# Kernel optimization log

Measured on AMD Instinct MI355X. Metric: run time of the kernel, lower is better.

Reference implementation:

```python
import jax, jax.numpy as jnp
import numpy as np

B, R, L_, K_, U_, E = 16, 32, 64, 16, 4, 64  # batch, realizations, APs, users, antennas, embed dim
C2 = 2 * U_                                   # input_dim_2 == output_dim == 2U
EPS = 1e-5


def _uniform(key, shape, fan_out, fan_in):
    # matches torch init: U(-ini, ini) with ini = sqrt(3/(out*in))
    ini = float(np.sqrt(3.0 / (fan_out * fan_in)))
    return jax.random.uniform(key, shape, jnp.float32, -ini, ini)


def setup_inputs() -> dict:
    key = jax.random.key(0)
    ks = jax.random.split(key, 12)
    return {
        "Hhat_real": jax.random.normal(ks[0], (B, R, L_, K_, U_), jnp.float32),
        "Hhat_imag": jax.random.normal(ks[1], (B, R, L_, K_, U_), jnp.float32),
        # layer 0 (hidden, out=E) -- note P3/P5 exist in torch but are unused in forward
        "P1_0": _uniform(ks[2], (E, E), E, E),
        "P2_0": _uniform(ks[3], (E, E), E, E),
        "P4_0": _uniform(ks[4], (E, C2), E, C2),
        "g0": jnp.ones((E,), jnp.float32),
        "b0": jnp.zeros((E,), jnp.float32),
        # layer 1 (hidden, out=E)
        "P1_1": _uniform(ks[5], (E, E), E, E),
        "P2_1": _uniform(ks[6], (E, E), E, E),
        "P4_1": _uniform(ks[7], (E, C2), E, C2),
        "g1": jnp.ones((E,), jnp.float32),
        "b1": jnp.zeros((E,), jnp.float32),
        # layer 2 (output, out=2U, no BN / no ReLU)
        "P1_2": _uniform(ks[8], (C2, E), C2, E),
        "P2_2": _uniform(ks[9], (C2, E), C2, E),
        "P4_2": _uniform(ks[10], (C2, C2), C2, C2),
        "nbrOfRealizations": R,
        "L": L_,
        "K": K_,
        "U": U_,
    }


def _layer(A, H, P1, P2, P4, gamma, beta, is_last):
    # A: [BR, C1, L, K], H: [BR, C2, L, K]
    A1 = jnp.einsum('oc,bclk->bolk', P1, A)
    A2 = jnp.einsum('oc,bcl->bol', P2, A.mean(-1))[:, :, :, None]   # mean over K
    A3 = jnp.einsum('oc,bck->bok', P2, A.mean(-2))[:, :, None, :]   # mean over L
    A4 = jnp.einsum('oc,bcl->bol', P4, H.mean(-1))[:, :, :, None]
    A5 = jnp.einsum('oc,bck->bok', P4, H.mean(-2))[:, :, None, :]
    out = 2 * A1 + 2 * A2 + 2 * A3 + 0.1 * A4 + 0.1 * A5
    if is_last:
        return out
    out = jax.nn.relu(out)
    # BatchNorm2d, training mode: biased variance over (batch, L, K)
    mu = out.mean((0, 2, 3), keepdims=True)
    var = ((out - mu) ** 2).mean((0, 2, 3), keepdims=True)
    return (out - mu) / jnp.sqrt(var + EPS) * gamma[None, :, None, None] + beta[None, :, None, None]


def reference(Hhat_real, Hhat_imag, P1_0, P2_0, P4_0, g0, b0,
              P1_1, P2_1, P4_1, g1, b1, P1_2, P2_2, P4_2,
              nbrOfRealizations, L, K, U):
    batch = Hhat_real.shape[0]
    BR = batch * nbrOfRealizations
    # [B,R,L,K,U] -> [BR,U,L,K] (real / imag channels), concat -> [BR, 2U, L, K]
    Hr = Hhat_real.reshape(BR, L, K, U).transpose(0, 3, 1, 2)
    Hi = Hhat_imag.reshape(BR, L, K, U).transpose(0, 3, 1, 2)
    Hup = jnp.concatenate([Hr, Hi], axis=1)
    A = jnp.zeros((BR, E, L, K), jnp.float32)  # V_AP_updated init
    A = _layer(A, Hup, P1_0, P2_0, P4_0, g0, b0, False)
    A = _layer(A, Hup, P1_1, P2_1, P4_1, g1, b1, False)
    V = _layer(A, Hup, P1_2, P2_2, P4_2, None, None, True)  # [BR, 2U, L, K]
    V = V.reshape(BR, 2, U, L, K)
    F1 = jnp.transpose(V[:, 0], (0, 2, 3, 1))  # [BR, L, K, U]
    F2 = jnp.transpose(V[:, 1], (0, 2, 3, 1))
    norm = jnp.sqrt((F1 ** 2).sum(-1) + (F2 ** 2).sum(-1))[..., None]
    Fhat = (F1 + 1j * F2) / norm
    return Fhat.reshape(batch, nbrOfRealizations, L, K, U)
```

## Files before the change

kernel.cpp:

```cpp
#include <hip/hip_runtime.h>
#include <math.h>

#define BRR 512
#define LLL 64
#define KKK 16
#define EEE 64
#define CC2 8
#define PPP 1024
#define BN_EPS 1e-5f
#define NSTRIPE 16

__device__ __forceinline__ float relu_f(float v){ return v>0.f?v:0.f; }
__device__ __forceinline__ int lds_row(int r){ return r*68 + (((r>>3)&7)<<2); }

#define OFF_HBL  0u
#define OFF_HBK  262144u
#define OFF_Y0   327680u
#define OFF_X1   851968u
#define OFF_Y1   2949120u
#define OFF_X2   3473408u
#define OFF_Y2   3735552u
#define OFF_M1L  3801088u
#define OFF_M1K  5898240u
#define OFF_SUM0 6422528u
#define OFF_SSQ0 6423552u
#define OFF_SUM1 6424576u
#define OFF_SSQ1 6425600u
#define OFF_S0   6426624u
#define OFF_T0   6426688u
#define OFF_S1   6426752u
#define OFF_T1   6426816u
#define WS_FLOATS 6426880u
#define OFF_M1KB 6426880u
#define OFF_T1S  6951168u
#define WS_BIG   40505600u

__global__ void k_zero(float4* __restrict__ p, int n4){
  int t = blockIdx.x*256 + threadIdx.x;
  if (t < n4) p[t] = make_float4(0.f,0.f,0.f,0.f);
}

__global__ __launch_bounds__(256) void k_prep(const float* __restrict__ Hr,
                                              const float* __restrict__ Hi,
                                              const float* __restrict__ P40,
                                              float* __restrict__ ws){
  __shared__ float sm[9344];
  int b = blockIdx.x, tid = threadIdx.x;
  const float* hrg = Hr + (size_t)b*4096;
  const float* hig = Hi + (size_t)b*4096;
  for (int t=tid;t<4096;t+=256){ sm[t]=hrg[t]; sm[4096+t]=hig[t]; }
  for (int t=tid;t<512;t+=256){ int c=t&63,j=t>>6; sm[8192+j*64+c]=P40[c*8+j]; }
  __syncthreads();
  for (int t=tid;t<512;t+=256){ int l=t>>3,c2=t&7;
    const float* src=sm+((c2<4)?0:4096); int u=c2&3;
    float s=0.f;
    #pragma unroll
    for(int k=0;k<16;++k) s+=src[(l*16+k)*4+u];
    sm[8704+t]=s*(1.f/16.f); }
  for (int t=tid;t<128;t+=256){ int k=t>>3,c2=t&7;
    const float* src=sm+((c2<4)?0:4096); int u=c2&3;
    float s=0.f;
    for(int l=0;l<64;++l) s+=src[(l*16+k)*4+u];
    sm[9216+t]=s*(1.f/64.f); }
  __syncthreads();
  for (int t=tid;t<1024;t+=256){ int k=t>>6,c=t&63; float s=0.f;
    #pragma unroll
    for(int j=0;j<8;++j) s+=sm[8192+j*64+c]*sm[9216+k*8+j];
    sm[4096+t]=0.1f*s; }
  for (int t=tid;t<4096;t+=256){ int l=t>>6,c=t&63; float s=0.f;
    #pragma unroll
    for(int j=0;j<8;++j) s+=sm[8192+j*64+c]*sm[8704+l*8+j];
    sm[t]=0.1f*s; }
  __syncthreads();
  for (int t=tid;t<1024;t+=256){ int c=t&63; float yv=sm[4096+t]; float s=0.f;
    for(int l=0;l<64;++l) s+=relu_f(sm[l*64+c]+yv);
    sm[5120+t]=s*(1.f/64.f); }
  float ssum=0.f, ssq=0.f;
  for (int t=tid;t<4096;t+=256){ int c=t&63; float xv=sm[t]; float s=0.f;
    #pragma unroll
    for(int k=0;k<16;++k){ float v=relu_f(xv+sm[4096+k*64+c]); s+=v; ssq+=v*v; }
    ssum+=s;
    ws[OFF_X1+(size_t)b*4096+t]=s*(1.f/16.f); }
  __syncthreads();
  sm[6144+tid]=ssum; sm[6400+tid]=ssq;
  __syncthreads();
  if (tid<64){
    float ts =sm[6144+tid]+sm[6208+tid]+sm[6272+tid]+sm[6336+tid];
    float tss=sm[6400+tid]+sm[6464+tid]+sm[6528+tid]+sm[6592+tid];
    int stripe = b & (NSTRIPE-1);
    atomicAdd(&ws[OFF_SUM0+stripe*64+tid], ts);
    atomicAdd(&ws[OFF_SSQ0+stripe*64+tid], tss);
  }
  for (int t=tid;t<512;t+=256)  ws[OFF_HBL+(size_t)b*512+t]=sm[8704+t];
  for (int t=tid;t<128;t+=256)  ws[OFF_HBK+(size_t)b*128+t]=sm[9216+t];
  for (int t=tid;t<1024;t+=256) ws[OFF_Y0+(size_t)b*1024+t]=sm[4096+t];
  for (int t=tid;t<1024;t+=256) ws[OFF_Y1+(size_t)b*1024+t]=sm[5120+t];
  for (int t=tid;t<4096;t+=256) ws[OFF_M1L+(size_t)b*4096+t]=sm[t];
}

__global__ void k_bn(float* __restrict__ ws, const float* __restrict__ g_,
                     const float* __restrict__ b_, unsigned sumOff, unsigned outOff){
  int tid = threadIdx.x;
  if (tid < 64){
    float s=0.f, ss=0.f;
    for (int i=0;i<NSTRIPE;++i){ s+=ws[sumOff+i*64+tid]; ss+=ws[sumOff+1024+i*64+tid]; }
    const float invN = 1.0f/((float)BRR*LLL*KKK);
    float mu=s*invN, var=ss*invN-mu*mu;
    float sc = g_[tid]/sqrtf(var+BN_EPS);
    ws[outOff+tid]=sc;
    ws[outOff+64+tid]=b_[tid]-mu*sc;
  }
}

__global__ __launch_bounds__(256) void k_xy1(float* __restrict__ ws,
                                             const float* __restrict__ P21,
                                             const float* __restrict__ P41){
  __shared__ float wt[4096], p41[512], mrow[1024], hbs[128], s0l[64], t0l[64];
  int bx = blockIdx.x, tid = threadIdx.x;
  for (int t=tid;t<4096;t+=256) wt[t] = 2.0f*P21[(t&63)*64 + (t>>6)];
  for (int t=tid;t<512;t+=256)  p41[t] = P41[t];
  if (tid<64){ s0l[tid]=ws[OFF_S0+tid]; t0l[tid]=ws[OFF_T0+tid]; }
  bool isX = bx < 2048;
  int row0 = isX ? bx*16 : (bx-2048)*16;
  if (isX){
    for (int t=tid;t<1024;t+=256) mrow[t] = ws[OFF_X1+(size_t)row0*64+t];
    if (tid<128) hbs[tid] = ws[OFF_HBL+(size_t)row0*8+tid];
  } else {
    for (int t=tid;t<1024;t+=256) mrow[t] = ws[OFF_Y1+(size_t)row0*64+t];
    if (tid<128) hbs[tid] = ws[OFF_HBK+(size_t)row0*8+tid];
  }
  __syncthreads();
  for (int t=tid;t<1024;t+=256){ int c=t&63; mrow[t]=s0l[c]*mrow[t]+t0l[c]; }
  __syncthreads();
  int r4 = tid>>6, o = tid&63;
  #pragma unroll
  for (int rr=0;rr<4;++rr){
    int rl = rr*4 + r4;
    float s=0.f;
    for (int c=0;c<64;++c) s += wt[c*64+o]*mrow[rl*64+c];
    float s2=0.f;
    #pragma unroll
    for (int j=0;j<8;++j) s2 += p41[o*8+j]*hbs[rl*8+j];
    float res = s + 0.1f*s2;
    if (isX) ws[OFF_X1+(size_t)(row0+rl)*64+o] = res;
    else     ws[OFF_Y1+(size_t)(row0+rl)*64+o] = res;
  }
}

#define T_W1   0
#define T_X08  4384
#define T_Y0   4896
#define T_X1   5984
#define T_Y1   6496
#define T_S0   7520
#define T_T0   7584
#define T_P4T0 7648
#define T_HB8  8160
#define T_END  8224

__device__ void t1_tile(float* sm, const float* __restrict__ ws,
                        const float* __restrict__ P11, const float* __restrict__ P40,
                        int b, int pblk, int tid,
                        float acc[8][4], int og, int pg, int lloc, int c0){
  for (int t=tid;t<4096;t+=256){ int o=t>>6,c=t&63; sm[T_W1+lds_row(o)+c]=2.0f*P11[t]; }
  for (int t=tid;t<1024;t+=256){ int k=t>>6,c=t&63; sm[T_Y0+k*68+c]=ws[OFF_Y0+(size_t)b*1024+t]; }
  for (int t=tid;t<512;t+=256)  sm[T_X1+t]=ws[OFF_X1+((size_t)b*64+pblk*8)*64+t];
  for (int t=tid;t<1024;t+=256) sm[T_Y1+t]=ws[OFF_Y1+(size_t)b*1024+t];
  for (int t=tid;t<512;t+=256){ int c=t&63,j=t>>6; sm[T_P4T0+j*64+c]=P40[c*8+j]; }
  if (tid<64){ sm[T_S0+tid]=ws[OFF_S0+tid]; sm[T_T0+tid]=ws[OFF_T0+tid]; }
  else if (tid<128){ int t2=tid-64; sm[T_HB8+t2]=ws[OFF_HBL+((size_t)b*64+pblk*8)*8+t2]; }
  __syncthreads();
  for (int e=tid;e<512;e+=256){ int l=e>>6,c=e&63; float s=0.f;
    #pragma unroll
    for(int j=0;j<8;++j) s += sm[T_P4T0+j*64+c]*sm[T_HB8+l*8+j];
    sm[T_X08+e]=0.1f*s; }
  __syncthreads();
  {
    float xb[8];
    *(float4*)&xb[0] = *(const float4*)&sm[T_X1 + lloc*64 + c0];
    *(float4*)&xb[4] = *(const float4*)&sm[T_X1 + lloc*64 + c0 + 4];
    #pragma unroll
    for (int i=0;i<4;++i){
      int k=(pg&3)*4+i;
      float yb[8];
      *(float4*)&yb[0] = *(const float4*)&sm[T_Y1 + k*64 + c0];
      *(float4*)&yb[4] = *(const float4*)&sm[T_Y1 + k*64 + c0 + 4];
      #pragma unroll
      for (int j=0;j<8;++j) acc[j][i]=xb[j]+yb[j];
    }
  }
  #pragma unroll 4
  for (int c4=0;c4<16;++c4){
    float4 xr  = *(const float4*)&sm[T_X08 + lloc*64 + c4*4];
    float4 s0v = *(const float4*)&sm[T_S0 + c4*4];
    float4 t0v = *(const float4*)&sm[T_T0 + c4*4];
    float4 aa[4];
    #pragma unroll
    for (int i=0;i<4;++i){
      int k=(pg&3)*4+i;
      float4 yr = *(const float4*)&sm[T_Y0 + k*68 + c4*4];
      aa[i].x = s0v.x*relu_f(xr.x+yr.x)+t0v.x;
      aa[i].y = s0v.y*relu_f(xr.y+yr.y)+t0v.y;
      aa[i].z = s0v.z*relu_f(xr.z+yr.z)+t0v.z;
      aa[i].w = s0v.w*relu_f(xr.w+yr.w)+t0v.w;
    }
    #pragma unroll
    for (int j=0;j<8;++j){
      float4 w = *(const float4*)&sm[T_W1 + lds_row(c0+j) + c4*4];
      #pragma unroll
      for (int i=0;i<4;++i)
        acc[j][i] += w.x*aa[i].x + w.y*aa[i].y + w.z*aa[i].z + w.w*aa[i].w;
    }
  }
  #pragma unroll
  for (int j=0;j<8;++j)
    #pragma unroll
    for (int i=0;i<4;++i) acc[j][i] = relu_f(acc[j][i]);
}

#define PD_W1   0
#define PD_Y0   4384
#define PD_Y1   5472
#define PD_X1D  6496
#define PD_X08D 7520
#define PD_CT   8544
#define PD_S0   8608
#define PD_T0   8672
#define PD_TOT  8736

__global__ __launch_bounds__(256) void k_pass1e(float* __restrict__ ws,
                                                const float* __restrict__ P11){
  __shared__ float sm[PD_TOT];
  int b = blockIdx.x >> 1, h = blockIdx.x & 1;
  int pb0 = h*4;
  int tid=threadIdx.x;
  int og=tid&7, pg=tid>>3, lloc=pg>>2, kg=pg&3, c0=og*8, wv=tid>>6;
  for (int t4=tid;t4<1024;t4+=256){ int o=t4>>4,c=(t4&15)*4;
    float4 v = *(const float4*)&P11[o*64+c];
    v.x*=2.f; v.y*=2.f; v.z*=2.f; v.w*=2.f;
    *(float4*)&sm[PD_W1+lds_row(o)+c]=v; }
  for (int t4=tid;t4<256;t4+=256){ int k=t4>>4,c=(t4&15)*4;
    float4 v = *(const float4*)&ws[OFF_Y0+(size_t)b*1024+t4*4];
    (void)k;
    *(float4*)&sm[PD_Y0+(t4>>4)*68+((t4&15)*4)]=v; }
  for (int t4=tid;t4<256;t4+=256)
    *(float4*)&sm[PD_Y1+t4*4] = *(const float4*)&ws[OFF_Y1+(size_t)b*1024+t4*4];
  if (tid<64){ sm[PD_S0+tid]=ws[OFF_S0+tid]; sm[PD_T0+tid]=ws[OFF_T0+tid]; }
  __syncthreads();
  if (tid<64){
    float ct=0.f;
    for (int c=0;c<64;++c) ct += sm[PD_W1+lds_row(tid)+c]*sm[PD_T0+c];
    sm[PD_CT+tid]=ct;
  }
  __syncthreads();
  for (int t4=tid;t4<1024;t4+=256){ int o=t4>>4,c=(t4&15)*4;
    float4 w = *(float4*)&sm[PD_W1+lds_row(o)+c];
    float4 s = *(const float4*)&sm[PD_S0+c];
    w.x*=s.x; w.y*=s.y; w.z*=s.z; w.w*=s.w;
    *(float4*)&sm[PD_W1+lds_row(o)+c]=w; }
  if (tid<128){
    float4 v1 = *(const float4*)&ws[OFF_X1 +((size_t)b*64+pb0*8)*64 + (size_t)tid*4];
    float4 v8 = *(const float4*)&ws[OFF_M1L+((size_t)b*64+pb0*8)*64 + (size_t)tid*4];
    *(float4*)&sm[PD_X1D  + tid*4] = v1;
    *(float4*)&sm[PD_X08D + tid*4] = v8;
  }
  float qsum[8], mk[8][4];
  #pragma unroll
  for (int j=0;j<8;++j){ qsum[j]=0.f;
    #pragma unroll
    for (int i=0;i<4;++i) mk[j][i]=0.f; }
  #pragma unroll 1
  for (int pp=0;pp<4;++pp){
    int pblk = pb0+pp;
    __syncthreads();
    if (pp<3 && tid<128){
      int pn = pblk+1;
      float4 v1 = *(const float4*)&ws[OFF_X1 +((size_t)b*64+pn*8)*64 + (size_t)tid*4];
      float4 v8 = *(const float4*)&ws[OFF_M1L+((size_t)b*64+pn*8)*64 + (size_t)tid*4];
      int bo = ((pp+1)&1)*512;
      *(float4*)&sm[PD_X1D  + bo + tid*4] = v1;
      *(float4*)&sm[PD_X08D + bo + tid*4] = v8;
    }
    int cb = (pp&1)*512;
    float acc[8][4];
    {
      float xb[8], ctv[8];
      *(float4*)&xb[0]  = *(const float4*)&sm[PD_X1D + cb + lloc*64 + c0];
      *(float4*)&xb[4]  = *(const float4*)&sm[PD_X1D + cb + lloc*64 + c0 + 4];
      *(float4*)&ctv[0] = *(const float4*)&sm[PD_CT + c0];
      *(float4*)&ctv[4] = *(const float4*)&sm[PD_CT + c0 + 4];
      #pragma unroll
      for (int i=0;i<4;++i){
        int k=kg*4+i;
        float yb[8];
        *(float4*)&yb[0] = *(const float4*)&sm[PD_Y1 + k*64 + c0];
        *(float4*)&yb[4] = *(const float4*)&sm[PD_Y1 + k*64 + c0 + 4];
        #pragma unroll
        for (int j=0;j<8;++j) acc[j][i]=xb[j]+yb[j]+ctv[j];
      }
    }
    #pragma unroll 4
    for (int c4=0;c4<16;++c4){
      float4 xr = *(const float4*)&sm[PD_X08D + cb + lloc*64 + c4*4];
      float4 aa[4];
      #pragma unroll
      for (int i=0;i<4;++i){
        int k=kg*4+i;
        float4 yr = *(const float4*)&sm[PD_Y0 + k*68 + c4*4];
        aa[i].x = relu_f(xr.x+yr.x);
        aa[i].y = relu_f(xr.y+yr.y);
        aa[i].z = relu_f(xr.z+yr.z);
        aa[i].w = relu_f(xr.w+yr.w);
      }
      #pragma unroll
      for (int j=0;j<8;++j){
        float4 w = *(const float4*)&sm[PD_W1 + lds_row(c0+j) + c4*4];
        #pragma unroll
        for (int i=0;i<4;++i)
          acc[j][i] += w.x*aa[i].x + w.y*aa[i].y + w.z*aa[i].z + w.w*aa[i].w;
      }
    }
    #pragma unroll
    for (int j=0;j<8;++j)
      #pragma unroll
      for (int i=0;i<4;++i) acc[j][i] = relu_f(acc[j][i]);
    {
      size_t tbase = OFF_T1S + ((size_t)b*8 + pblk)*8192 + (size_t)tid*4;
      #pragma unroll
      for (int j=0;j<8;++j)
        *(float4*)&ws[tbase + j*1024] =
          make_float4(acc[j][0],acc[j][1],acc[j][2],acc[j][3]);
    }
    float sj[8];
    #pragma unroll
    for (int j=0;j<8;++j){
      sj[j]=acc[j][0]+acc[j][1]+acc[j][2]+acc[j][3];
      qsum[j]+=acc[j][0]*acc[j][0]+acc[j][1]*acc[j][1]+acc[j][2]*acc[j][2]+acc[j][3]*acc[j][3];
      #pragma unroll
      for (int i=0;i<4;++i) mk[j][i]+=acc[j][i];
    }
    #pragma unroll
    for (int j=0;j<8;++j){
      float r=sj[j];
      r += __shfl_xor(r, 8, 64);
      r += __shfl_xor(r, 16, 64);
      sj[j]=r;
    }
    if (kg==0){
      const float inv16 = 1.f/16.f;
      float4 v0 = make_float4(sj[0]*inv16, sj[1]*inv16, sj[2]*inv16, sj[3]*inv16);
      float4 v1 = make_float4(sj[4]*inv16, sj[5]*inv16, sj[6]*inv16, sj[7]*inv16);
      size_t base = OFF_M1L + ((size_t)b*64 + pblk*8 + lloc)*64 + c0;
      *(float4*)&ws[base]   = v0;
      *(float4*)&ws[base+4] = v1;
    }
  }
  __syncthreads();
  #pragma unroll
  for (int j=0;j<8;++j){
    #pragma unroll
    for (int i=0;i<4;++i){
      float v = mk[j][i] + __shfl_xor(mk[j][i], 32, 64);
      if ((tid & 32)==0)
        sm[wv*1088 + (og*4+kg)*33 + i*8 + j] = v;
    }
  }
  #pragma unroll
  for (int j=0;j<8;++j) sm[4384+(c0+j)*33+pg] = qsum[j];
  __syncthreads();
  unsigned mko = h ? OFF_M1KB : OFF_M1K;
  float tsacc=0.f;
  #pragma unroll
  for (int r=0;r<4;++r){
    int e = tid + r*256;
    int k=e>>6, c=e&63;
    int a = ((c>>3)*4+(k>>2))*33 + (k&3)*8 + (c&7);
    float v = sm[a]+sm[1088+a]+sm[2176+a]+sm[3264+a];
    tsacc += v;
    ws[mko+(size_t)b*1024+e] = v*(1.f/64.f);
  }
  sm[6496 + (tid&63)*5 + wv] = tsacc;
  __syncthreads();
  if (tid<64){
    float ts  = sm[6496+tid*5+0]+sm[6496+tid*5+1]+sm[6496+tid*5+2]+sm[6496+tid*5+3];
    float tss = 0.f;
    for (int g=0; g<32; ++g) tss += sm[4384+tid*33+g];
    int stripe = b & (NSTRIPE-1);
    atomicAdd(&ws[OFF_SUM1+stripe*64+tid], ts);
    atomicAdd(&ws[OFF_SSQ1+stripe*64+tid], tss);
  }
}

#define MK_OFF 8224
__global__ __launch_bounds__(256) void k_pass1(float* __restrict__ ws,
                                               const float* __restrict__ P11,
                                               const float* __restrict__ P40){
  __shared__ float sm[12576];
  int b=blockIdx.x, tid=threadIdx.x;
  int og=tid&7, pg=tid>>3, lloc=pg>>2, kg=pg&3, c0=og*8, wv=tid>>6;
  for (int t=tid;t<4096;t+=256){ int o=t>>6,c=t&63; sm[T_W1+lds_row(o)+c]=2.0f*P11[t]; }
  for (int t=tid;t<1024;t+=256){ int k=t>>6,c=t&63; sm[T_Y0+k*68+c]=ws[OFF_Y0+(size_t)b*1024+t]; }
  for (int t=tid;t<1024;t+=256) sm[T_Y1+t]=ws[OFF_Y1+(size_t)b*1024+t];
  for (int t=tid;t<512;t+=256){ int c=t&63,j=t>>6; sm[T_P4T0+j*64+c]=P40[c*8+j]; }
  if (tid<64){ sm[T_S0+tid]=ws[OFF_S0+tid]; sm[T_T0+tid]=ws[OFF_T0+tid]; }
  for (int t=tid;t<4352;t+=256) sm[MK_OFF+t]=0.f;
  float qsum[8];
  #pragma unroll
  for (int j=0;j<8;++j) qsum[j]=0.f;
  #pragma unroll 1
  for (int pblk=0;pblk<8;++pblk){
    __syncthreads();
    for (int t=tid;t<512;t+=256) sm[T_X1+t]=ws[OFF_X1+((size_t)b*64+pblk*8)*64+t];
    if (tid<64) sm[T_HB8+tid]=ws[OFF_HBL+((size_t)b*64+pblk*8)*8+tid];
    __syncthreads();
    for (int e=tid;e<512;e+=256){ int l=e>>6,c=e&63; float s=0.f;
      #pragma unroll
      for(int j=0;j<8;++j) s += sm[T_P4T0+j*64+c]*sm[T_HB8+l*8+j];
      sm[T_X08+e]=0.1f*s; }
    __syncthreads();
    float acc[8][4];
    {
      float xb[8];
      *(float4*)&xb[0] = *(const float4*)&sm[T_X1 + lloc*64 + c0];
      *(float4*)&xb[4] = *(const float4*)&sm[T_X1 + lloc*64 + c0 + 4];
      #pragma unroll
      for (int i=0;i<4;++i){
        int k=kg*4+i;
        float yb[8];
        *(float4*)&yb[0] = *(const float4*)&sm[T_Y1 + k*64 + c0];
        *(float4*)&yb[4] = *(const float4*)&sm[T_Y1 + k*64 + c0 + 4];
        #pragma unroll
        for (int j=0;j<8;++j) acc[j][i]=xb[j]+yb[j];
      }
    }
    #pragma unroll 4
    for (int c4=0;c4<16;++c4){
      float4 xr  = *(const float4*)&sm[T_X08 + lloc*64 + c4*4];
      float4 s0v = *(const float4*)&sm[T_S0 + c4*4];
      float4 t0v = *(const float4*)&sm[T_T0 + c4*4];
      float4 aa[4];
      #pragma unroll
      for (int i=0;i<4;++i){
        int k=kg*4+i;
        float4 yr = *(const float4*)&sm[T_Y0 + k*68 + c4*4];
        aa[i].x = s0v.x*relu_f(xr.x+yr.x)+t0v.x;
        aa[i].y = s0v.y*relu_f(xr.y+yr.y)+t0v.y;
        aa[i].z = s0v.z*relu_f(xr.z+yr.z)+t0v.z;
        aa[i].w = s0v.w*relu_f(xr.w+yr.w)+t0v.w;
      }
      #pragma unroll
      for (int j=0;j<8;++j){
        float4 w = *(const float4*)&sm[T_W1 + lds_row(c0+j) + c4*4];
        #pragma unroll
        for (int i=0;i<4;++i)
          acc[j][i] += w.x*aa[i].x + w.y*aa[i].y + w.z*aa[i].z + w.w*aa[i].w;
      }
    }
    #pragma unroll
    for (int j=0;j<8;++j)
      #pragma unroll
      for (int i=0;i<4;++i) acc[j][i] = relu_f(acc[j][i]);
    float sj[8];
    #pragma unroll
    for (int j=0;j<8;++j){
      sj[j]=acc[j][0]+acc[j][1]+acc[j][2]+acc[j][3];
      qsum[j]+=acc[j][0]*acc[j][0]+acc[j][1]*acc[j][1]+acc[j][2]*acc[j][2]+acc[j][3]*acc[j][3];
    }
    #pragma unroll
    for (int j=0;j<8;++j){
      float r=sj[j];
      r += __shfl_xor(r, 8, 64);
      r += __shfl_xor(r, 16, 64);
      sj[j]=r;
    }
    if (kg==0){
      const float inv16 = 1.f/16.f;
      float4 v0 = make_float4(sj[0]*inv16, sj[1]*inv16, sj[2]*inv16, sj[3]*inv16);
      float4 v1 = make_float4(sj[4]*inv16, sj[5]*inv16, sj[6]*inv16, sj[7]*inv16);
      size_t base = OFF_M1L + ((size_t)b*64 + pblk*8 + lloc)*64 + c0;
      *(float4*)&ws[base]   = v0;
      *(float4*)&ws[base+4] = v1;
    }
    #pragma unroll
    for (int j=0;j<8;++j){
      #pragma unroll
      for (int i=0;i<4;++i){
        float v = acc[j][i] + __shfl_xor(acc[j][i], 32, 64);
        if ((tid & 32)==0)
          sm[MK_OFF + wv*1088 + (og*4+kg)*33 + i*8 + j] += v;
      }
    }
  }
  __syncthreads();
  float tsacc=0.f;
  #pragma unroll
  for (int r=0;r<4;++r){
    int e = tid + r*256;
    int k=e>>6, c=e&63;
    int a = ((c>>3)*4+(k>>2))*33 + (k&3)*8 + (c&7);
    float v = sm[MK_OFF+a]+sm[MK_OFF+1088+a]+sm[MK_OFF+2176+a]+sm[MK_OFF+3264+a];
    tsacc += v;
    ws[OFF_M1K+(size_t)b*1024+e] = v*(1.f/64.f);
  }
  __syncthreads();
  sm[8224 + (tid&63)*5 + wv] = tsacc;
  #pragma unroll
  for (int j=0;j<8;++j) sm[8544+(c0+j)*33+pg] = qsum[j];
  __syncthreads();
  if (tid<64){
    float ts  = sm[8224+tid*5+0]+sm[8224+tid*5+1]+sm[8224+tid*5+2]+sm[8224+tid*5+3];
    float tss = 0.f;
    for (int g=0; g<32; ++g) tss += sm[8544+tid*33+g];
    int stripe = b & (NSTRIPE-1);
    atomicAdd(&ws[OFF_SUM1+stripe*64+tid], ts);
    atomicAdd(&ws[OFF_SSQ1+stripe*64+tid], tss);
  }
}

__global__ __launch_bounds__(256) void k_xy2s(float* __restrict__ ws,
                                              const float* __restrict__ P22,
                                              const float* __restrict__ P42,
                                              int two){
  __shared__ float mln[4352];
  __shared__ float mkn[1088];
  __shared__ float w2[512];
  __shared__ float p42s[64];
  __shared__ float hbl[512];
  __shared__ float hbk[128];
  __shared__ float s1l[64], t1l[64];
  int b = blockIdx.x, tid = threadIdx.x;
  if (tid<64){ s1l[tid]=ws[OFF_S1+tid]; t1l[tid]=ws[OFF_T1+tid]; }
  for (int t=tid;t<512;t+=256) w2[t] = 2.0f*P22[(t&7)*64 + (t>>3)];
  if (tid<64) p42s[tid] = P42[tid];
  for (int t=tid;t<512;t+=256) hbl[t] = ws[OFF_HBL+(size_t)b*512+t];
  if (tid<128) hbk[tid] = ws[OFF_HBK+(size_t)b*128+tid];
  __syncthreads();
  for (int t=tid;t<4096;t+=256){ int l=t>>6,c=t&63;
    mln[l*68+c] = s1l[c]*ws[OFF_M1L+(size_t)b*4096+t] + t1l[c]; }
  for (int t=tid;t<1024;t+=256){ int k=t>>6,c=t&63;
    float mv = ws[OFF_M1K+(size_t)b*1024+t];
    if (two) mv += ws[OFF_M1KB+(size_t)b*1024+t];
    mkn[k*68+c] = s1l[c]*mv + t1l[c]; }
  __syncthreads();
  for (int t=tid;t<512;t+=256){
    int l=t>>3, o2=t&7;
    float s=0.f;
    for (int c=0;c<64;++c) s += w2[c*8+o2]*mln[l*68+c];
    float s2=0.f;
    #pragma unroll
    for (int j=0;j<8;++j) s2 += p42s[o2*8+j]*hbl[l*8+j];
    ws[OFF_X2+(size_t)b*512+t] = s + 0.1f*s2;
  }
  if (tid<128){
    int k=tid>>3, o2=tid&7;
    float s=0.f;
    for (int c=0;c<64;++c) s += w2[c*8+o2]*mkn[k*68+c];
    float s2=0.f;
    #pragma unroll
    for (int j=0;j<8;++j) s2 += p42s[o2*8+j]*hbk[k*8+j];
    ws[OFF_Y2+(size_t)b*128+tid] = s + 0.1f*s2;
  }
}

__device__ __forceinline__ void final_epilogue(const float* __restrict__ ws,
                                               float* sm, int b, int pblk, int tid,
                                               float* __restrict__ out,
                                               long long out_cap, int interleaved){
  if (tid < 128){
    int p = tid, k = p & 15, lglob = pblk*8 + (p>>4);
    float a2[8];
    {
      const float* xp = ws + OFF_X2 + ((size_t)b*64+lglob)*8;
      const float* yp = ws + OFF_Y2 + ((size_t)b*16+k)*8;
      float4 x0_ = *(const float4*)&xp[0];
      float4 x1_ = *(const float4*)&xp[4];
      float4 y0_ = *(const float4*)&yp[0];
      float4 y1_ = *(const float4*)&yp[4];
      a2[0]=x0_.x+y0_.x; a2[1]=x0_.y+y0_.y; a2[2]=x0_.z+y0_.z; a2[3]=x0_.w+y0_.w;
      a2[4]=x1_.x+y1_.x; a2[5]=x1_.y+y1_.y; a2[6]=x1_.z+y1_.z; a2[7]=x1_.w+y1_.w;
    }
    for (int c=0;c<64;++c){
      float tn = sm[9028+c]*sm[c*133 + (c>>3) + p] + sm[9092+c];
      #pragma unroll
      for (int o2=0;o2<8;++o2) a2[o2] += sm[8516+o2*64+c]*tn;
    }
    float nrm=0.f;
    #pragma unroll
    for (int o2=0;o2<8;++o2) nrm += a2[o2]*a2[o2];
    float inv = 1.0f/sqrtf(nrm);
    size_t pos = (size_t)b*PPP + lglob*KKK + k;
    if (interleaved){
      long long idx = (long long)pos*8;
      if (idx+8 <= out_cap){
        *(float4*)&out[idx]   = make_float4(a2[0]*inv, a2[4]*inv, a2[1]*inv, a2[5]*inv);
        *(float4*)&out[idx+4] = make_float4(a2[2]*inv, a2[6]*inv, a2[3]*inv, a2[7]*inv);
      }
    } else {
      long long idx = (long long)pos*4;
      if (idx+4 <= out_cap)
        *(float4*)&out[idx] = make_float4(a2[0]*inv, a2[1]*inv, a2[2]*inv, a2[3]*inv);
    }
  }
}

__global__ __launch_bounds__(256) void k_final_big(const float* __restrict__ ws,
                                                   const float* __restrict__ P12,
                                                   float* __restrict__ out,
                                                   long long out_cap, int interleaved){
  __shared__ float sm[9156];
  int bid=blockIdx.x, b=bid>>3, pblk=bid&7, tid=threadIdx.x;
  for (int t=tid;t<512;t+=256) sm[8516+t] = 2.0f*P12[t];
  if (tid<64) sm[9028+tid]=ws[OFF_S1+tid];
  else if (tid<128) sm[9092+(tid-64)]=ws[OFF_T1+(tid-64)];
  {
    size_t base = OFF_T1S + ((size_t)b*8 + pblk)*8192;
    for (int t4=tid;t4<2048;t4+=256){
      float4 v = *(const float4*)&ws[base + (size_t)t4*4];
      int j = t4>>8, lane = t4&255;
      int c = (lane&7)*8 + j;
      int pb = (lane>>5)*16 + ((lane>>3)&3)*4;
      int o = c*133 + (c>>3) + pb;
      sm[o+0]=v.x; sm[o+1]=v.y; sm[o+2]=v.z; sm[o+3]=v.w;
    }
  }
  __syncthreads();
  int half = tid>>7, p = tid&127;
  int k = p & 15, lglob = pblk*8 + (p>>4);
  float a2[8];
  if (half==0){
    const float* xp = ws + OFF_X2 + ((size_t)b*64+lglob)*8;
    const float* yp = ws + OFF_Y2 + ((size_t)b*16+k)*8;
    float4 x0_ = *(const float4*)&xp[0];
    float4 x1_ = *(const float4*)&xp[4];
    float4 y0_ = *(const float4*)&yp[0];
    float4 y1_ = *(const float4*)&yp[4];
    a2[0]=x0_.x+y0_.x; a2[1]=x0_.y+y0_.y; a2[2]=x0_.z+y0_.z; a2[3]=x0_.w+y0_.w;
    a2[4]=x1_.x+y1_.x; a2[5]=x1_.y+y1_.y; a2[6]=x1_.z+y1_.z; a2[7]=x1_.w+y1_.w;
  } else {
    #pragma unroll
    for (int o2=0;o2<8;++o2) a2[o2]=0.f;
  }
  int cb = half*32;
  for (int cc=0;cc<32;++cc){
    int c = cb+cc;
    float tn = sm[9028+c]*sm[c*133 + (c>>3) + p] + sm[9092+c];
    #pragma unroll
    for (int o2=0;o2<8;++o2) a2[o2] += sm[8516+o2*64+c]*tn;
  }
  __syncthreads();
  if (half==1){
    #pragma unroll
    for (int o2=0;o2<8;++o2) sm[p*9+o2] = a2[o2];
  }
  __syncthreads();
  if (half==0){
    #pragma unroll
    for (int o2=0;o2<8;++o2) a2[o2] += sm[p*9+o2];
    float nrm=0.f;
    #pragma unroll
    for (int o2=0;o2<8;++o2) nrm += a2[o2]*a2[o2];
    float inv = 1.0f/sqrtf(nrm);
    size_t pos = (size_t)b*PPP + lglob*KKK + k;
    if (interleaved){
      long long idx = (long long)pos*8;
      if (idx+8 <= out_cap){
        *(float4*)&out[idx]   = make_float4(a2[0]*inv, a2[4]*inv, a2[1]*inv, a2[5]*inv);
        *(float4*)&out[idx+4] = make_float4(a2[2]*inv, a2[6]*inv, a2[3]*inv, a2[7]*inv);
      }
    } else {
      long long idx = (long long)pos*4;
      if (idx+4 <= out_cap)
        *(float4*)&out[idx] = make_float4(a2[0]*inv, a2[1]*inv, a2[2]*inv, a2[3]*inv);
    }
  }
}

__global__ __launch_bounds__(256) void k_final(const float* __restrict__ ws,
                                               const float* __restrict__ P11,
                                               const float* __restrict__ P40,
                                               const float* __restrict__ P12,
                                               float* __restrict__ out,
                                               long long out_cap, int interleaved){
  __shared__ float sm[9156];
  int bid=blockIdx.x, b=bid>>3, pblk=bid&7, tid=threadIdx.x;
  int og=tid&7, pg=tid>>3, lloc=pg>>2, c0=og*8;
  for (int t=tid;t<512;t+=256) sm[8516+t] = 2.0f*P12[t];
  if (tid<64) sm[9028+tid]=ws[OFF_S1+tid];
  else if (tid<128) sm[9092+(tid-64)]=ws[OFF_T1+(tid-64)];
  float acc[8][4];
  t1_tile(sm, ws, P11, P40, b, pblk, tid, acc, og, pg, lloc, c0);
  __syncthreads();
  {
    int kg = pg&3;
    #pragma unroll
    for (int i=0;i<4;++i){
      int p = lloc*16 + kg*4 + i;
      #pragma unroll
      for (int j=0;j<8;++j) sm[(c0+j)*133 + og + p] = acc[j][i];
    }
  }
  __syncthreads();
  final_epilogue(ws, sm, b, pblk, tid, out, out_cap, interleaved);
}

extern "C" void kernel_launch(void* const* d_in, const int* in_sizes, int n_in,
                              void* d_out, int out_size, void* d_ws, size_t ws_size,
                              hipStream_t stream) {
  if (n_in < 15) return;
  if (in_sizes[0] != BRR*4096 || in_sizes[1] != BRR*4096) return;
  if (in_sizes[4] != 512)  return;
  if (in_sizes[7] != 4096) return;
  if (in_sizes[12] != 512) return;
  if (ws_size < (size_t)WS_FLOATS*4) return;

  const float* Hr   = (const float*)d_in[0];
  const float* Hi   = (const float*)d_in[1];
  const float* P4_0 = (const float*)d_in[4];
  const float* g0   = (const float*)d_in[5];
  const float* b0   = (const float*)d_in[6];
  const float* P1_1 = (const float*)d_in[7];
  const float* P2_1 = (const float*)d_in[8];
  const float* P4_1 = (const float*)d_in[9];
  const float* g1   = (const float*)d_in[10];
  const float* b1   = (const float*)d_in[11];
  const float* P1_2 = (const float*)d_in[12];
  const float* P2_2 = (const float*)d_in[13];
  const float* P4_2 = (const float*)d_in[14];
  float* ws  = (float*)d_ws;
  float* out = (float*)d_out;
  int interleaved = (out_size >= 4194304) ? 1 : 0;
  int big = (ws_size >= (size_t)WS_BIG*4) ? 1 : 0;

  k_zero<<<4, 256, 0, stream>>>((float4*)(ws + OFF_SUM0), 4096/4);
  k_prep<<<BRR, 256, 0, stream>>>(Hr, Hi, P4_0, ws);
  k_bn<<<1, 64, 0, stream>>>(ws, g0, b0, OFF_SUM0, OFF_S0);
  k_xy1<<<2560, 256, 0, stream>>>(ws, P2_1, P4_1);
  if (big) k_pass1e<<<BRR*2, 256, 0, stream>>>(ws, P1_1);
  else     k_pass1<<<BRR, 256, 0, stream>>>(ws, P1_1, P4_0);
  k_bn<<<1, 64, 0, stream>>>(ws, g1, b1, OFF_SUM1, OFF_S1);
  k_xy2s<<<BRR, 256, 0, stream>>>(ws, P2_2, P4_2, big);
  if (big) k_final_big<<<BRR*8, 256, 0, stream>>>(ws, P1_2, out,
                                                  (long long)out_size, interleaved);
  else     k_final<<<BRR*8, 256, 0, stream>>>(ws, P1_1, P4_0, P1_2, out,
                                              (long long)out_size, interleaved);
}
```

Before: 300.0 us.

## Process two L-blocks per iteration in pass1 to reuse weight and Y0 loads

The pass-1 kernel now computes two position blocks at once, sharing each LDS load of the W1 row and the Y0 row between both accumulator sets. Prefetch changes from a per-iteration double buffer to loading two blocks up front and staging the next pair in registers, which halves the loop trips and barriers. The cost is double the accumulator registers (64 floats plus the aa arrays), which may lower occupancy or cause spills, and the unroll factor drops from 4 to 2.

Result: faster. 284.5 us (-5.2%).

```diff
diff --git a/kernel.cpp b/kernel.cpp
--- a/kernel.cpp
+++ b/kernel.cpp
@@ -228,24 +228,30 @@
 #define PD_T0   8672
 #define PD_TOT  8736
 
-__global__ __launch_bounds__(256) void k_pass1e(float* __restrict__ ws,
+__global__ __launch_bounds__(256) void k_pass1f(float* __restrict__ ws,
                                                 const float* __restrict__ P11){
   __shared__ float sm[PD_TOT];
   int b = blockIdx.x >> 1, h = blockIdx.x & 1;
   int pb0 = h*4;
   int tid=threadIdx.x;
-  int og=tid&7, pg=tid>>3, lloc=pg>>2, kg=pg&3, c0=og*8, wv=tid>>6;
+  int og=tid&7, kg=(tid>>3)&3, lloc=tid>>5, c0=og*8, wv=tid>>6;
   for (int t4=tid;t4<1024;t4+=256){ int o=t4>>4,c=(t4&15)*4;
     float4 v = *(const float4*)&P11[o*64+c];
     v.x*=2.f; v.y*=2.f; v.z*=2.f; v.w*=2.f;
     *(float4*)&sm[PD_W1+lds_row(o)+c]=v; }
-  for (int t4=tid;t4<256;t4+=256){ int k=t4>>4,c=(t4&15)*4;
+  for (int t4=tid;t4<256;t4+=256){
     float4 v = *(const float4*)&ws[OFF_Y0+(size_t)b*1024+t4*4];
-    (void)k;
     *(float4*)&sm[PD_Y0+(t4>>4)*68+((t4&15)*4)]=v; }
   for (int t4=tid;t4<256;t4+=256)
     *(float4*)&sm[PD_Y1+t4*4] = *(const float4*)&ws[OFF_Y1+(size_t)b*1024+t4*4];
   if (tid<64){ sm[PD_S0+tid]=ws[OFF_S0+tid]; sm[PD_T0+tid]=ws[OFF_T0+tid]; }
+  {
+    int po = tid>>7, idx = tid&127;
+    float4 v1 = *(const float4*)&ws[OFF_X1 +((size_t)b*64+(pb0+po)*8)*64 + (size_t)idx*4];
+    float4 v8 = *(const float4*)&ws[OFF_M1L+((size_t)b*64+(pb0+po)*8)*64 + (size_t)idx*4];
+    *(float4*)&sm[PD_X1D  + po*512 + idx*4] = v1;
+    *(float4*)&sm[PD_X08D + po*512 + idx*4] = v8;
+  }
   __syncthreads();
   if (tid<64){
     float ct=0.f;
@@ -258,35 +264,28 @@
     float4 s = *(const float4*)&sm[PD_S0+c];
     w.x*=s.x; w.y*=s.y; w.z*=s.z; w.w*=s.w;
     *(float4*)&sm[PD_W1+lds_row(o)+c]=w; }
-  if (tid<128){
-    float4 v1 = *(const float4*)&ws[OFF_X1 +((size_t)b*64+pb0*8)*64 + (size_t)tid*4];
-    float4 v8 = *(const float4*)&ws[OFF_M1L+((size_t)b*64+pb0*8)*64 + (size_t)tid*4];
-    *(float4*)&sm[PD_X1D  + tid*4] = v1;
-    *(float4*)&sm[PD_X08D + tid*4] = v8;
-  }
   float qsum[8], mk[8][4];
   #pragma unroll
   for (int j=0;j<8;++j){ qsum[j]=0.f;
     #pragma unroll
     for (int i=0;i<4;++i) mk[j][i]=0.f; }
   #pragma unroll 1
-  for (int pp=0;pp<4;++pp){
-    int pblk = pb0+pp;
+  for (int pr=0;pr<2;++pr){
+    int pblkA = pb0 + 2*pr, pblkB = pblkA + 1;
     __syncthreads();
-    if (pp<3 && tid<128){
-      int pn = pblk+1;
-      float4 v1 = *(const float4*)&ws[OFF_X1 +((size_t)b*64+pn*8)*64 + (size_t)tid*4];
-      float4 v8 = *(const float4*)&ws[OFF_M1L+((size_t)b*64+pn*8)*64 + (size_t)tid*4];
-      int bo = ((pp+1)&1)*512;
-      *(float4*)&sm[PD_X1D  + bo + tid*4] = v1;
-      *(float4*)&sm[PD_X08D + bo + tid*4] = v8;
-    }
-    int cb = (pp&1)*512;
-    float acc[8][4];
+    float4 n1, n8;
+    if (pr==0){
+      int po = tid>>7, idx = tid&127, pn = pb0 + 2 + po;
+      n1 = *(const float4*)&ws[OFF_X1 +((size_t)b*64+pn*8)*64 + (size_t)idx*4];
+      n8 = *(const float4*)&ws[OFF_M1L+((size_t)b*64+pn*8)*64 + (size_t)idx*4];
+    }
+    float accA[8][4], accB[8][4];
     {
-      float xb[8], ctv[8];
-      *(float4*)&xb[0]  = *(const float4*)&sm[PD_X1D + cb + lloc*64 + c0];
-      *(float4*)&xb[4]  = *(const float4*)&sm[PD_X1D + cb + lloc*64 + c0 + 4];
+      float xbA[8], xbB[8], ctv[8];
+      *(float4*)&xbA[0] = *(const float4*)&sm[PD_X1D       + lloc*64 + c0];
+      *(float4*)&xbA[4] = *(const float4*)&sm[PD_X1D       + lloc*64 + c0 + 4];
+      *(float4*)&xbB[0] = *(const float4*)&sm[PD_X1D + 512 + lloc*64 + c0];
+      *(float4*)&xbB[4] = *(const float4*)&sm[PD_X1D + 512 + lloc*64 + c0 + 4];
       *(float4*)&ctv[0] = *(const float4*)&sm[PD_CT + c0];
       *(float4*)&ctv[4] = *(const float4*)&sm[PD_CT + c0 + 4];
       #pragma unroll
@@ -296,63 +295,90 @@
         *(float4*)&yb[0] = *(const float4*)&sm[PD_Y1 + k*64 + c0];
         *(float4*)&yb[4] = *(const float4*)&sm[PD_Y1 + k*64 + c0 + 4];
         #pragma unroll
-        for (int j=0;j<8;++j) acc[j][i]=xb[j]+yb[j]+ctv[j];
-      }
-    }
-    #pragma unroll 4
+        for (int j=0;j<8;++j){
+          float base = yb[j]+ctv[j];
+          accA[j][i]=xbA[j]+base;
+          accB[j][i]=xbB[j]+base;
+        }
+      }
+    }
+    #pragma unroll 2
     for (int c4=0;c4<16;++c4){
-      float4 xr = *(const float4*)&sm[PD_X08D + cb + lloc*64 + c4*4];
-      float4 aa[4];
+      float4 xrA = *(const float4*)&sm[PD_X08D       + lloc*64 + c4*4];
+      float4 xrB = *(const float4*)&sm[PD_X08D + 512 + lloc*64 + c4*4];
+      float4 aaA[4], aaB[4];
       #pragma unroll
       for (int i=0;i<4;++i){
         int k=kg*4+i;
         float4 yr = *(const float4*)&sm[PD_Y0 + k*68 + c4*4];
-        aa[i].x = relu_f(xr.x+yr.x);
-        aa[i].y = relu_f(xr.y+yr.y);
-        aa[i].z = relu_f(xr.z+yr.z);
-        aa[i].w = relu_f(xr.w+yr.w);
+        aaA[i].x = relu_f(xrA.x+yr.x); aaB[i].x = relu_f(xrB.x+yr.x);
+        aaA[i].y = relu_f(xrA.y+yr.y); aaB[i].y = relu_f(xrB.y+yr.y);
+        aaA[i].z = relu_f(xrA.z+yr.z); aaB[i].z = relu_f(xrB.z+yr.z);
+        aaA[i].w = relu_f(xrA.w+yr.w); aaB[i].w = relu_f(xrB.w+yr.w);
       }
       #pragma unroll
       for (int j=0;j<8;++j){
         float4 w = *(const float4*)&sm[PD_W1 + lds_row(c0+j) + c4*4];
         #pragma unroll
-        for (int i=0;i<4;++i)
-          acc[j][i] += w.x*aa[i].x + w.y*aa[i].y + w.z*aa[i].z + w.w*aa[i].w;
+        for (int i=0;i<4;++i){
+          accA[j][i] += w.x*aaA[i].x + w.y*aaA[i].y + w.z*aaA[i].z + w.w*aaA[i].w;
+          accB[j][i] += w.x*aaB[i].x + w.y*aaB[i].y + w.z*aaB[i].z + w.w*aaB[i].w;
+        }
       }
     }
     #pragma unroll
     for (int j=0;j<8;++j)
       #pragma unroll
-      for (int i=0;i<4;++i) acc[j][i] = relu_f(acc[j][i]);
+      for (int i=0;i<4;++i){
+        accA[j][i] = relu_f(accA[j][i]);
+        accB[j][i] = relu_f(accB[j][i]);
+      }
     {
-      size_t tbase = OFF_T1S + ((size_t)b*8 + pblk)*8192 + (size_t)tid*4;
-      #pragma unroll
-      for (int j=0;j<8;++j)
-        *(float4*)&ws[tbase + j*1024] =
-          make_float4(acc[j][0],acc[j][1],acc[j][2],acc[j][3]);
-    }
-    float sj[8];
+      size_t tbA = OFF_T1S + ((size_t)b*8 + pblkA)*8192 + (size_t)tid*4;
+      size_t tbB = OFF_T1S + ((size_t)b*8 + pblkB)*8192 + (size_t)tid*4;
+      #pragma unroll
+      for (int j=0;j<8;++j){
+        *(float4*)&ws[tbA + j*1024] =
+          make_float4(accA[j][0],accA[j][1],accA[j][2],accA[j][3]);
+        *(float4*)&ws[tbB + j*1024] =
+          make_float4(accB[j][0],accB[j][1],accB[j][2],accB[j][3]);
+      }
+    }
+    float sjA[8], sjB[8];
     #pragma unroll
     for (int j=0;j<8;++j){
-      sj[j]=acc[j][0]+acc[j][1]+acc[j][2]+acc[j][3];
-      qsum[j]+=acc[j][0]*acc[j][0]+acc[j][1]*acc[j][1]+acc[j][2]*acc[j][2]+acc[j][3]*acc[j][3];
-      #pragma unroll
-      for (int i=0;i<4;++i) mk[j][i]+=acc[j][i];
+      sjA[j]=accA[j][0]+accA[j][1]+accA[j][2]+accA[j][3];
+      sjB[j]=accB[j][0]+accB[j][1]+accB[j][2]+accB[j][3];
+      qsum[j]+=accA[j][0]*accA[j][0]+accA[j][1]*accA[j][1]+accA[j][2]*accA[j][2]+accA[j][3]*accA[j][3];
+      qsum[j]+=accB[j][0]*accB[j][0]+accB[j][1]*accB[j][1]+accB[j][2]*accB[j][2]+accB[j][3]*accB[j][3];
+      #pragma unroll
+      for (int i=0;i<4;++i) mk[j][i]+=accA[j][i]+accB[j][i];
     }
     #pragma unroll
     for (int j=0;j<8;++j){
-      float r=sj[j];
-      r += __shfl_xor(r, 8, 64);
-      r += __shfl_xor(r, 16, 64);
-      sj[j]=r;
+      float rA=sjA[j];
+      rA += __shfl_xor(rA, 8, 64);
+      rA += __shfl_xor(rA, 16, 64);
+      sjA[j]=rA;
+      float rB=sjB[j];
+      rB += __shfl_xor(rB, 8, 64);
+      rB += __shfl_xor(rB, 16, 64);
+      sjB[j]=rB;
     }
     if (kg==0){
       const float inv16 = 1.f/16.f;
-      float4 v0 = make_float4(sj[0]*inv16, sj[1]*inv16, sj[2]*inv16, sj[3]*inv16);
-      float4 v1 = make_float4(sj[4]*inv16, sj[5]*inv16, sj[6]*inv16, sj[7]*inv16);
-      size_t base = OFF_M1L + ((size_t)b*64 + pblk*8 + lloc)*64 + c0;
-      *(float4*)&ws[base]   = v0;
-      *(float4*)&ws[base+4] = v1;
+      size_t baseA = OFF_M1L + ((size_t)b*64 + pblkA*8 + lloc)*64 + c0;
+      size_t baseB = OFF_M1L + ((size_t)b*64 + pblkB*8 + lloc)*64 + c0;
+      *(float4*)&ws[baseA]   = make_float4(sjA[0]*inv16, sjA[1]*inv16, sjA[2]*inv16, sjA[3]*inv16);
+      *(float4*)&ws[baseA+4] = make_float4(sjA[4]*inv16, sjA[5]*inv16, sjA[6]*inv16, sjA[7]*inv16);
+      *(float4*)&ws[baseB]   = make_float4(sjB[0]*inv16, sjB[1]*inv16, sjB[2]*inv16, sjB[3]*inv16);
+      *(float4*)&ws[baseB+4] = make_float4(sjB[4]*inv16, sjB[5]*inv16, sjB[6]*inv16, sjB[7]*inv16);
+    }
+    if (pr==0){
+      __syncthreads();
+      int po = tid>>7, idx = tid&127;
+      *(float4*)&sm[PD_X1D  + po*512 + idx*4] = n1;
+      *(float4*)&sm[PD_X08D + po*512 + idx*4] = n8;
     }
   }
   __syncthreads();
@@ -365,8 +391,11 @@
         sm[wv*1088 + (og*4+kg)*33 + i*8 + j] = v;
     }
   }
-  #pragma unroll
-  for (int j=0;j<8;++j) sm[4384+(c0+j)*33+pg] = qsum[j];
+  {
+    int pg = tid>>3;
+    #pragma unroll
+    for (int j=0;j<8;++j) sm[4384+(c0+j)*33+pg] = qsum[j];
+  }
   __syncthreads();
   unsigned mko = h ? OFF_M1KB : OFF_M1K;
   float tsacc=0.f;
@@ -735,7 +764,7 @@
   k_prep<<<BRR, 256, 0, stream>>>(Hr, Hi, P4_0, ws);
   k_bn<<<1, 64, 0, stream>>>(ws, g0, b0, OFF_SUM0, OFF_S0);
   k_xy1<<<2560, 256, 0, stream>>>(ws, P2_1, P4_1);
-  if (big) k_pass1e<<<BRR*2, 256, 0, stream>>>(ws, P1_1);
+  if (big) k_pass1f<<<BRR*2, 256, 0, stream>>>(ws, P1_1);
   else     k_pass1<<<BRR, 256, 0, stream>>>(ws, P1_1, P4_0);
   k_bn<<<1, 64, 0, stream>>>(ws, g1, b1, OFF_SUM1, OFF_S1);
   k_xy2s<<<BRR, 256, 0, stream>>>(ws, P2_2, P4_2, big);
```
